# Optimization experiments

Hardware: AMD Instinct MI355X
Metric: run time of the kernel (lower is better)

## Reference

```python
import jax, jax.numpy as jnp
import numpy as np

DIM = 256
MUL = 4
NUM_ENTRIES = 64
B, K = 16, 64
R = MUL * DIM


def setup_inputs() -> dict:
    key = jax.random.key(0)
    k_slots, k_idx, k_w1, k_w2 = jax.random.split(key, 4)
    slots = jax.random.normal(k_slots, (B, K, DIM), dtype=jnp.float32)
    indices = jax.random.randint(k_idx, (B, K), 0, NUM_ENTRIES, dtype=jnp.int64)
    # xavier_normal: std = sqrt(2 / (fan_in + fan_out)) over last two dims
    std1 = float(np.sqrt(2.0 / (DIM + R)))
    std2 = float(np.sqrt(2.0 / (R + DIM)))
    w1 = jax.random.normal(k_w1, (NUM_ENTRIES, DIM, R), dtype=jnp.float32) * std1
    w2 = jax.random.normal(k_w2, (NUM_ENTRIES, R, DIM), dtype=jnp.float32) * std2
    b1 = jnp.zeros((NUM_ENTRIES, R), dtype=jnp.float32)
    b2 = jnp.zeros((NUM_ENTRIES, DIM), dtype=jnp.float32)
    return {"slots": slots, "w1": w1, "b1": b1, "w2": w2, "b2": b2, "indices": indices}


def reference(slots, w1, b1, w2, b2, indices):
    # gather per-(b,k) expert weights, then 2-layer MLP (matvec per slot)
    h = jnp.einsum('bkd,bkdr->bkr', slots, w1[indices]) + b1[indices]  # (B,K,R)
    h = jax.nn.relu(h)
    out = jnp.einsum('bkr,bkrd->bkd', h, w2[indices]) + b2[indices]    # (B,K,DIM)
    return out
```

## Files before the change

kernel.cpp:

```cpp
#include <hip/hip_runtime.h>
#include <stdint.h>

#define DIMC 256
#define RTOT 1024
#define NE 64
#define NSLOT 1024
#define RC 256
#define TILE 32
#define SG 8
#define DT 32
#define NT 16

typedef const __attribute__((address_space(1))) void* gptr_t;
typedef __attribute__((address_space(3))) void* lptr_t;

__global__ __launch_bounds__(1024) void bucket_kernel(
    const int* __restrict__ idx, int* __restrict__ count,
    int* __restrict__ start, int* __restrict__ list) {
  __shared__ int cnt[NE];
  __shared__ int offs[NE];
  __shared__ int cur[NE];
  int t = threadIdx.x;
  if (t < NE) cnt[t] = 0;
  __syncthreads();
  int e = idx[t] & (NE - 1);
  atomicAdd(&cnt[e], 1);
  __syncthreads();
  if (t == 0) {
    int acc = 0;
    for (int i = 0; i < NE; ++i) { offs[i] = acc; cur[i] = acc; acc += cnt[i]; }
  }
  __syncthreads();
  if (t < NE) { count[t] = cnt[t]; start[t] = offs[t]; }
  int pos = atomicAdd(&cur[e], 1);
  list[pos] = t;
}

static __device__ __forceinline__ float4 f4ma(float a, float4 w, float4 c) {
  c.x = fmaf(a, w.x, c.x);
  c.y = fmaf(a, w.y, c.y);
  c.z = fmaf(a, w.z, c.z);
  c.w = fmaf(a, w.w, c.w);
  return c;
}

__global__ __launch_bounds__(256) void mlp_kernel(
    const float* __restrict__ slots, const float* __restrict__ w1,
    const float* __restrict__ b1, const float* __restrict__ w2,
    const float* __restrict__ b2, const int* __restrict__ count,
    const int* __restrict__ start, const int* __restrict__ list,
    float* __restrict__ out) {
  const int rc = blockIdx.x;
  const int e  = blockIdx.y;
  const int n  = count[e];
  if (n == 0) return;
  const int t  = threadIdx.x;
  const int g4 = t & 63;
  const int w  = t >> 6;
  const int rbase = rc * RC;

  __shared__ float xs[TILE][DIMC];
  __shared__ float wt[2][DT][DIMC];
  __shared__ int   sid[TILE];

  const float* w1e = w1 + (size_t)e * DIMC * RTOT + rbase + g4 * 4;
  const float* w2e = w2 + ((size_t)e * RTOT + rbase) * DIMC + g4 * 4;

  const float4 b1v = *(const float4*)&b1[e * RTOT + rbase + g4 * 4];
  const float4 b2v = (rc == 0) ? *(const float4*)&b2[e * DIMC + g4 * 4]
                               : make_float4(0.f, 0.f, 0.f, 0.f);
  const int st = start[e];

  for (int s0 = 0; s0 < n; s0 += TILE) {
    const int m = (n - s0 < TILE) ? (n - s0) : TILE;

    __syncthreads();
    if (t < TILE) sid[t] = list[st + s0 + ((t < m) ? t : (m - 1))];
    __syncthreads();

#pragma unroll
    for (int j = 0; j < DT / 4; ++j) {
      int row = w * (DT / 4) + j;
      __builtin_amdgcn_global_load_lds((gptr_t)(w1e + (size_t)row * RTOT),
                                       (lptr_t)&wt[0][row][0], 16, 0, 0);
    }
    for (int i = t; i < TILE * (DIMC / 4); i += 256) {
      int s = i >> 6, d4 = i & 63;
      *(float4*)&xs[s][d4 * 4] =
          ((const float4*)slots)[(size_t)sid[s] * (DIMC / 4) + d4];
    }
    __syncthreads();

    float4 acc[SG];
#pragma unroll
    for (int s = 0; s < SG; ++s) acc[s] = b1v;

    for (int k = 0; k < NT; ++k) {
      const int buf = k & 1;

      if (k + 1 < NT) {
        const int kn = k + 1;
        const float* src = (kn < 8) ? (w1e + (size_t)(kn * DT) * RTOT)
                                    : (w2e + (size_t)((kn - 8) * DT) * DIMC);
        const size_t rstride = (kn < 8) ? RTOT : DIMC;
#pragma unroll
        for (int j = 0; j < DT / 4; ++j) {
          int row = w * (DT / 4) + j;
          __builtin_amdgcn_global_load_lds((gptr_t)(src + (size_t)row * rstride),
                                           (lptr_t)&wt[buf ^ 1][row][0], 16, 0, 0);
        }
      }

      if (k == 8) {
#pragma unroll
        for (int s = 0; s < SG; ++s) {
          float4 h = acc[s];
          h.x = fmaxf(h.x, 0.f); h.y = fmaxf(h.y, 0.f);
          h.z = fmaxf(h.z, 0.f); h.w = fmaxf(h.w, 0.f);
          *(float4*)&xs[w * SG + s][g4 * 4] = h;
          acc[s] = b2v;
        }
        __syncthreads();
      }

      const int xoff = (k < 8 ? k : k - 8) * DT;
#pragma unroll
      for (int dg = 0; dg < DT / 4; ++dg) {
        float4 wA = *(const float4*)&wt[buf][dg * 4 + 0][g4 * 4];
        float4 wB = *(const float4*)&wt[buf][dg * 4 + 1][g4 * 4];
        float4 wC = *(const float4*)&wt[buf][dg * 4 + 2][g4 * 4];
        float4 wD = *(const float4*)&wt[buf][dg * 4 + 3][g4 * 4];
#pragma unroll
        for (int s = 0; s < SG; ++s) {
          float4 xv = *(const float4*)&xs[w * SG + s][xoff + dg * 4];
          acc[s] = f4ma(xv.x, wA, acc[s]);
          acc[s] = f4ma(xv.y, wB, acc[s]);
          acc[s] = f4ma(xv.z, wC, acc[s]);
          acc[s] = f4ma(xv.w, wD, acc[s]);
        }
      }
      __syncthreads();
    }

#pragma unroll
    for (int s = 0; s < SG; ++s) {
      int ss = w * SG + s;
      if (ss < m) {
        float* po = &out[(size_t)sid[ss] * DIMC + g4 * 4];
        atomicAdd(po + 0, acc[s].x);
        atomicAdd(po + 1, acc[s].y);
        atomicAdd(po + 2, acc[s].z);
        atomicAdd(po + 3, acc[s].w);
      }
    }
  }
}

extern "C" void kernel_launch(void* const* d_in, const int* in_sizes, int n_in,
                              void* d_out, int out_size, void* d_ws, size_t ws_size,
                              hipStream_t stream) {
  const float* slots   = (const float*)d_in[0];
  const float* w1      = (const float*)d_in[1];
  const float* b1      = (const float*)d_in[2];
  const float* w2      = (const float*)d_in[3];
  const float* b2      = (const float*)d_in[4];
  const int*   indices = (const int*)d_in[5];
  float* out = (float*)d_out;

  int* ws    = (int*)d_ws;
  int* count = ws;
  int* start = ws + 64;
  int* list  = ws + 128;

  hipMemsetAsync(d_out, 0, (size_t)out_size * sizeof(float), stream);
  bucket_kernel<<<1, NSLOT, 0, stream>>>(indices, count, start, list);
  mlp_kernel<<<dim3(4, NE), 256, 0, stream>>>(slots, w1, b1, w2, b2,
                                              count, start, list, out);
}
```

Baseline: 184.2 us.

## Split reduction dimension across wave pairs and skip padded slot rows

Waves are now paired. Each pair splits the 32-row weight chunk into two 16-row halves, and the two pair groups split the actual slot count rather than fixed groups of 8. Partial sums from the second half-wave are combined through shared memory before the ReLU and before the final atomic adds. Padded slots beyond the real count are no longer loaded or computed, which targets experts with few tokens (about 16 on average). The cost is a larger per-thread accumulator array (16 float4), which raises register pressure, plus extra shared-memory exchanges and barriers.

Result: slower. 202.9 us (+10.2%).

```diff
diff --git a/kernel.cpp b/kernel.cpp
--- a/kernel.cpp
+++ b/kernel.cpp
@@ -7,9 +7,9 @@
 #define NSLOT 1024
 #define RC 256
 #define TILE 32
-#define SG 8
 #define DT 32
 #define NT 16
+#define HMAX 16
 
 typedef const __attribute__((address_space(1))) void* gptr_t;
 typedef __attribute__((address_space(3))) void* lptr_t;
@@ -57,6 +57,8 @@
   const int t  = threadIdx.x;
   const int g4 = t & 63;
   const int w  = t >> 6;
+  const int rh = w & 1;
+  const int sh = w >> 1;
   const int rbase = rc * RC;
 
   __shared__ float xs[TILE][DIMC];
@@ -66,16 +68,19 @@
   const float* w1e = w1 + (size_t)e * DIMC * RTOT + rbase + g4 * 4;
   const float* w2e = w2 + ((size_t)e * RTOT + rbase) * DIMC + g4 * 4;
 
-  const float4 b1v = *(const float4*)&b1[e * RTOT + rbase + g4 * 4];
-  const float4 b2v = (rc == 0) ? *(const float4*)&b2[e * DIMC + g4 * 4]
-                               : make_float4(0.f, 0.f, 0.f, 0.f);
+  const float4 zero4 = make_float4(0.f, 0.f, 0.f, 0.f);
+  const float4 b1v = (rh == 0) ? *(const float4*)&b1[e * RTOT + rbase + g4 * 4] : zero4;
+  const float4 b2v = (rh == 0 && rc == 0) ? *(const float4*)&b2[e * DIMC + g4 * 4] : zero4;
   const int st = start[e];
 
   for (int s0 = 0; s0 < n; s0 += TILE) {
-    const int m = (n - s0 < TILE) ? (n - s0) : TILE;
-
-    __syncthreads();
-    if (t < TILE) sid[t] = list[st + s0 + ((t < m) ? t : (m - 1))];
+    const int m   = (n - s0 < TILE) ? (n - s0) : TILE;
+    const int mh0 = (m + 1) >> 1;
+    const int sbase = sh * mh0;
+    const int mh  = sh ? (m - mh0) : mh0;
+
+    __syncthreads();
+    if (t < m) sid[t] = list[st + s0 + t];
     __syncthreads();
 
 #pragma unroll
@@ -84,19 +89,44 @@
       __builtin_amdgcn_global_load_lds((gptr_t)(w1e + (size_t)row * RTOT),
                                        (lptr_t)&wt[0][row][0], 16, 0, 0);
     }
-    for (int i = t; i < TILE * (DIMC / 4); i += 256) {
+    for (int i = t; i < m * (DIMC / 4); i += 256) {
       int s = i >> 6, d4 = i & 63;
       *(float4*)&xs[s][d4 * 4] =
           ((const float4*)slots)[(size_t)sid[s] * (DIMC / 4) + d4];
     }
     __syncthreads();
 
-    float4 acc[SG];
-#pragma unroll
-    for (int s = 0; s < SG; ++s) acc[s] = b1v;
+    float4 acc[HMAX];
+#pragma unroll
+    for (int s = 0; s < HMAX; ++s) acc[s] = b1v;
 
     for (int k = 0; k < NT; ++k) {
       const int buf = k & 1;
+
+      if (k == 8) {
+        if (rh == 1) {
+#pragma unroll
+          for (int s = 0; s < HMAX; ++s)
+            if (s < mh) *(float4*)&xs[sbase + s][g4 * 4] = acc[s];
+        }
+        __syncthreads();
+        if (rh == 0) {
+#pragma unroll
+          for (int s = 0; s < HMAX; ++s)
+            if (s < mh) {
+              float4 p = *(const float4*)&xs[sbase + s][g4 * 4];
+              float4 h;
+              h.x = fmaxf(acc[s].x + p.x, 0.f);
+              h.y = fmaxf(acc[s].y + p.y, 0.f);
+              h.z = fmaxf(acc[s].z + p.z, 0.f);
+              h.w = fmaxf(acc[s].w + p.w, 0.f);
+              *(float4*)&xs[sbase + s][g4 * 4] = h;
+            }
+        }
+        __syncthreads();
+#pragma unroll
+        for (int s = 0; s < HMAX; ++s) acc[s] = b2v;
+      }
 
       if (k + 1 < NT) {
         const int kn = k + 1;
@@ -111,47 +141,44 @@
         }
       }
 
-      if (k == 8) {
-#pragma unroll
-        for (int s = 0; s < SG; ++s) {
-          float4 h = acc[s];
-          h.x = fmaxf(h.x, 0.f); h.y = fmaxf(h.y, 0.f);
-          h.z = fmaxf(h.z, 0.f); h.w = fmaxf(h.w, 0.f);
-          *(float4*)&xs[w * SG + s][g4 * 4] = h;
-          acc[s] = b2v;
-        }
-        __syncthreads();
-      }
-
-      const int xoff = (k < 8 ? k : k - 8) * DT;
-#pragma unroll
-      for (int dg = 0; dg < DT / 4; ++dg) {
-        float4 wA = *(const float4*)&wt[buf][dg * 4 + 0][g4 * 4];
-        float4 wB = *(const float4*)&wt[buf][dg * 4 + 1][g4 * 4];
-        float4 wC = *(const float4*)&wt[buf][dg * 4 + 2][g4 * 4];
-        float4 wD = *(const float4*)&wt[buf][dg * 4 + 3][g4 * 4];
-#pragma unroll
-        for (int s = 0; s < SG; ++s) {
-          float4 xv = *(const float4*)&xs[w * SG + s][xoff + dg * 4];
-          acc[s] = f4ma(xv.x, wA, acc[s]);
-          acc[s] = f4ma(xv.y, wB, acc[s]);
-          acc[s] = f4ma(xv.z, wC, acc[s]);
-          acc[s] = f4ma(xv.w, wD, acc[s]);
-        }
+      const int xoff = ((k < 8) ? k : (k - 8)) * DT + rh * 16;
+#pragma unroll
+      for (int dg = 0; dg < 4; ++dg) {
+        const int row = rh * 16 + dg * 4;
+        float4 wA = *(const float4*)&wt[buf][row + 0][g4 * 4];
+        float4 wB = *(const float4*)&wt[buf][row + 1][g4 * 4];
+        float4 wC = *(const float4*)&wt[buf][row + 2][g4 * 4];
+        float4 wD = *(const float4*)&wt[buf][row + 3][g4 * 4];
+#pragma unroll
+        for (int s = 0; s < HMAX; ++s)
+          if (s < mh) {
+            float4 xv = *(const float4*)&xs[sbase + s][xoff + dg * 4];
+            acc[s] = f4ma(xv.x, wA, acc[s]);
+            acc[s] = f4ma(xv.y, wB, acc[s]);
+            acc[s] = f4ma(xv.z, wC, acc[s]);
+            acc[s] = f4ma(xv.w, wD, acc[s]);
+          }
       }
       __syncthreads();
     }
 
-#pragma unroll
-    for (int s = 0; s < SG; ++s) {
-      int ss = w * SG + s;
-      if (ss < m) {
-        float* po = &out[(size_t)sid[ss] * DIMC + g4 * 4];
-        atomicAdd(po + 0, acc[s].x);
-        atomicAdd(po + 1, acc[s].y);
-        atomicAdd(po + 2, acc[s].z);
-        atomicAdd(po + 3, acc[s].w);
-      }
+    if (rh == 1) {
+#pragma unroll
+      for (int s = 0; s < HMAX; ++s)
+        if (s < mh) *(float4*)&xs[sbase + s][g4 * 4] = acc[s];
+    }
+    __syncthreads();
+    if (rh == 0) {
+#pragma unroll
+      for (int s = 0; s < HMAX; ++s)
+        if (s < mh) {
+          float4 p = *(const float4*)&xs[sbase + s][g4 * 4];
+          float* po = &out[(size_t)sid[sbase + s] * DIMC + g4 * 4];
+          atomicAdd(po + 0, acc[s].x + p.x);
+          atomicAdd(po + 1, acc[s].y + p.y);
+          atomicAdd(po + 2, acc[s].z + p.z);
+          atomicAdd(po + 3, acc[s].w + p.w);
+        }
     }
   }
 }
```
